# Optimization experiments

Measured on AMD Instinct MI355X. Metric: run time of the kernel, lower is better.

## Reference

```python
import jax, jax.numpy as jnp
import numpy as np

B, S, F, H = 64, 2048, 1024, 1024


def setup_inputs() -> dict:
    key = jax.random.key(0)
    k0, k1, k2, k3, k4 = jax.random.split(key, 5)
    scale = 1.0 / np.sqrt(H)
    return {
        "inputs": jax.random.normal(k0, (B, S, F), jnp.float32),
        "hidden_state": jnp.zeros((B, H), jnp.float32),
        "W_ih": jax.random.uniform(k1, (H, F), jnp.float32, -scale, scale),
        "W_hh": jax.random.uniform(k2, (H, H), jnp.float32, -scale, scale),
        "b_ih": jax.random.uniform(k3, (H,), jnp.float32, -scale, scale),
        "b_hh": jax.random.uniform(k4, (H,), jnp.float32, -scale, scale),
        "chunk_len": 128,
        "chunk_stride": 128,
    }


def reference(inputs, hidden_state, W_ih, W_hh, b_ih, b_hh, chunk_len, chunk_stride):
    # ReverseRNNLayer with chunk_stride == chunk_len and S % chunk_len == 0:
    # each chunk starts from a zeroed hidden state (incl. the first chunk) and is
    # scanned in reverse time order; outputs are collected per index then the
    # whole list is reversed, yielding chunks in reverse chunk order with
    # ascending time order inside each chunk.
    b_, S_, F_ = inputs.shape
    H_ = W_hh.shape[0]
    L = chunk_len
    NC = S_ // L
    # (B, NC, L, F) -> reversed time within chunk -> (L, B*NC, F)
    xc = inputs.reshape(b_, NC, L, F_)
    xr = jnp.flip(xc, axis=2).transpose(2, 0, 1, 3).reshape(L, b_ * NC, F_)
    # precompute input projection outside the scan (hoists the big GEMM)
    xproj = xr @ W_ih.T + (b_ih + b_hh)  # (L, B*NC, H)

    def step(h, xp):
        h = jnp.tanh(xp + h @ W_hh.T)
        return h, h

    h0 = jnp.zeros((b_ * NC, H_), inputs.dtype)
    h_last, ys = jax.lax.scan(step, h0, xproj)  # ys: (L, B*NC, H), reversed time
    ys = jnp.flip(ys, axis=0)                   # ascending time within chunk
    ys = ys.reshape(L, b_, NC, H_).transpose(1, 2, 0, 3)  # (B, NC, L, H)
    ys = jnp.flip(ys, axis=1).reshape(b_, S_, H_)  # chunks in reverse chunk order
    # final hidden state = carry after processing the LAST chunk
    h_final = h_last.reshape(b_, NC, H_)[:, NC - 1]
    return ys, h_final
```

## Files before the change

kernel.cpp:

```cpp
#include <hip/hip_runtime.h>
#include <hip/hip_bf16.h>
#include <stdint.h>

typedef __bf16 bf16x8 __attribute__((ext_vector_type(8)));
typedef float f32x4 __attribute__((ext_vector_type(4)));

#define Bb 64
#define Ss 2048
#define Ff 1024
#define Hh 1024
#define Ll 128
#define NCc 16

__device__ __forceinline__ uint16_t f2bf_rne(float x) {
    union { float f; uint32_t u; } c; c.f = x;
    uint32_t u = c.u;
    return (uint16_t)((u + 0x7FFFu + ((u >> 16) & 1u)) >> 16);
}

__device__ __forceinline__ void load_lds16(const void* g, void* l) {
    __builtin_amdgcn_global_load_lds(
        (__attribute__((address_space(1))) void*)(uintptr_t)g,
        (__attribute__((address_space(3))) void*)l, 16, 0, 0);
}

__global__ __launch_bounds__(256) void prep_kernel(
    const float* __restrict__ Wih, const float* __restrict__ Whh,
    const float* __restrict__ bih, const float* __restrict__ bhh,
    uint16_t* __restrict__ wih_bf, uint16_t* __restrict__ whh_bf,
    uint16_t* __restrict__ h0, float* __restrict__ bias,
    unsigned* __restrict__ bar)
{
    int i = blockIdx.x * 256 + threadIdx.x;
    wih_bf[i] = f2bf_rne(Wih[i]);
    whh_bf[i] = f2bf_rne(Whh[i]);
    h0[i] = 0;
    if (i < Hh) bias[i] = bih[i] + bhh[i];
    if (i < 1024) bar[i] = 0u;
}

__global__ __launch_bounds__(256) void xproj_kernel(
    const float* __restrict__ x, const uint16_t* __restrict__ wih,
    const float* __restrict__ bias, float* __restrict__ out)
{
    __shared__ __bf16 As[128*32];
    __shared__ __bf16 Bs[128*32];
    const int hb = blockIdx.y & 7;
    const int mb = blockIdx.x * 128 + (blockIdx.y >> 3);
    const int tid = threadIdx.x;
    const int wave = tid >> 6, lane = tid & 63;
    const int wm = (wave >> 1) * 64, wn = (wave & 1) * 64;

    const int t  = mb >> 3;
    const int n0 = (mb & 7) * 128;

    int arow[4], acol[4];
#pragma unroll
    for (int p = 0; p < 4; ++p) {
        int idx = p*256 + tid;
        int r = idx >> 3, c4 = idx & 7;
        int n = n0 + r;
        int b = n >> 4, c = n & 15;
        arow[p] = b*Ss + c*Ll + (Ll-1-t);
        acol[p] = c4*4;
    }

    f32x4 acc[4][4] = {};

    for (int k0 = 0; k0 < Ff; k0 += 32) {
        __syncthreads();
#pragma unroll
        for (int p = 0; p < 2; ++p) {
            int idx = p*256 + tid;
            int r = idx >> 2, c = idx & 3;
            load_lds16(wih + (size_t)(hb*128 + r)*1024 + (k0 + c*8), (char*)Bs + idx*16);
        }
#pragma unroll
        for (int p = 0; p < 4; ++p) {
            int idx = p*256 + tid;
            const float4 v = *(const float4*)(x + (size_t)arow[p]*Ff + k0 + acol[p]);
            uint32_t lo = (uint32_t)f2bf_rne(v.x) | ((uint32_t)f2bf_rne(v.y) << 16);
            uint32_t hi = (uint32_t)f2bf_rne(v.z) | ((uint32_t)f2bf_rne(v.w) << 16);
            *(uint2*)((char*)As + idx*8) = make_uint2(lo, hi);
        }
        __syncthreads();

        bf16x8 af[4], bfr[4];
#pragma unroll
        for (int i = 0; i < 4; ++i)
            af[i] = *(const bf16x8*)&As[(wm + i*16 + (lane & 15))*32 + (lane >> 4)*8];
#pragma unroll
        for (int j = 0; j < 4; ++j)
            bfr[j] = *(const bf16x8*)&Bs[(wn + j*16 + (lane & 15))*32 + (lane >> 4)*8];
#pragma unroll
        for (int i = 0; i < 4; ++i)
#pragma unroll
            for (int j = 0; j < 4; ++j)
                acc[i][j] = __builtin_amdgcn_mfma_f32_16x16x32_bf16(af[i], bfr[j], acc[i][j], 0, 0, 0);
    }

    float bsv[4]; int coln[4];
#pragma unroll
    for (int j = 0; j < 4; ++j) {
        coln[j] = hb*128 + wn + j*16 + (lane & 15);
        bsv[j] = bias[coln[j]];
    }
#pragma unroll
    for (int i = 0; i < 4; ++i) {
#pragma unroll
        for (int r = 0; r < 4; ++r) {
            int n = n0 + wm + i*16 + (lane >> 4)*4 + r;
            int b = n >> 4, c = n & 15;
            size_t orow = (size_t)b*Ss + (size_t)(NCc-1-c)*Ll + (Ll-1-t);
            float* orp = out + orow*Hh;
#pragma unroll
            for (int j = 0; j < 4; ++j)
                orp[coln[j]] = acc[i][j][r] + bsv[j];
        }
    }
}


__device__ __forceinline__ void stage_A(const uint16_t* __restrict__ hp, int nb, int c,
                                        __bf16* dst, int tid) {
#pragma unroll
    for (int p = 0; p < 2; ++p) {
        int u = p*256 + tid;
        int r = u >> 3;
        int s = u & 7;
        int k = (c << 6) + ((s ^ (r & 7)) << 3);
        load_lds16(hp + ((size_t)(nb*64 + r) << 10) + k, (char*)dst + u*16);
    }
}

__global__ __launch_bounds__(256, 1) void scan_kernel(
    const uint16_t* __restrict__ whh,
    uint16_t* __restrict__ h0buf, uint16_t* __restrict__ h1buf,
    float* __restrict__ out, unsigned* __restrict__ bar)
{
    __shared__ __align__(16) __bf16 Bs[64 * 1024];
    __shared__ __align__(16) __bf16 As[2][64 * 64];

    const int bid = blockIdx.x;
    const int nb = bid & 15;
    const int hb = bid >> 4;
    const int tid = threadIdx.x;
    const int lane = tid & 63;
    const int wave = tid >> 6;
    const int wm = (wave >> 1) * 32, wn = (wave & 1) * 32;
    const int l15 = lane & 15, l4 = lane >> 4;

    unsigned* cnt = bar + nb * 64;
    unsigned* gen = bar + nb * 64 + 32;

    for (int u = tid; u < 8192; u += 256) {
        int r = u >> 7, s = u & 127;
        int k = (s ^ (r & 7)) << 3;
        bf16x8 v = *(const bf16x8*)(whh + ((size_t)(hb*64 + r) << 10) + k);
        *(bf16x8*)((char*)Bs + u*16) = v;
    }

    float* orb[2][4];
    int hoff[2][4];
#pragma unroll
    for (int i = 0; i < 2; ++i)
#pragma unroll
        for (int r = 0; r < 4; ++r) {
            int n = nb*64 + wm + l4*4 + i*16 + r;
            int b = n >> 4, cch = n & 15;
            orb[i][r] = out + ((size_t)b*Ss + (size_t)(NCc-1-cch)*Ll)*Hh + hb*64;
            hoff[i][r] = n*Hh + hb*64;
        }

    __syncthreads();

#pragma unroll 1
    for (int t = 0; t < Ll; ++t) {
        const uint16_t* hp = (t & 1) ? h1buf : h0buf;
        uint16_t*       hn = (t & 1) ? h0buf : h1buf;
        const size_t toff = (size_t)(Ll-1-t) * Hh;

        float xpv[2][4][2];
#pragma unroll
        for (int i = 0; i < 2; ++i)
#pragma unroll
            for (int r = 0; r < 4; ++r) {
                const float* orp = orb[i][r] + toff;
                xpv[i][r][0] = orp[wn + l15];
                xpv[i][r][1] = orp[wn + 16 + l15];
            }

        f32x4 acc[2][2] = {};

        if (t > 0) {
            stage_A(hp, nb, 0, &As[0][0], tid);
            __syncthreads();
#pragma unroll
            for (int c = 0; c < 16; ++c) {
                if (c < 15) stage_A(hp, nb, c + 1, &As[(c + 1) & 1][0], tid);
                const char* Ab = (const char*)&As[c & 1][0];
#pragma unroll
                for (int ks = 0; ks < 2; ++ks) {
                    bf16x8 af[2], bv[2];
#pragma unroll
                    for (int i = 0; i < 2; ++i) {
                        int r = wm + i*16 + l15;
                        int off = r*128 + ((ks*64 + l4*16) ^ ((r & 7) << 4));
                        af[i] = *(const bf16x8*)(Ab + off);
                    }
#pragma unroll
                    for (int j = 0; j < 2; ++j) {
                        int r = wn + j*16 + l15;
                        int off = r*2048 + ((c*128 + ks*64 + l4*16) ^ ((r & 7) << 4));
                        bv[j] = *(const bf16x8*)((const char*)Bs + off);
                    }
#pragma unroll
                    for (int i = 0; i < 2; ++i)
#pragma unroll
                        for (int j = 0; j < 2; ++j)
                            acc[i][j] = __builtin_amdgcn_mfma_f32_16x16x32_bf16(af[i], bv[j], acc[i][j], 0, 0, 0);
                }
                __syncthreads();
            }
        }

#pragma unroll
        for (int i = 0; i < 2; ++i)
#pragma unroll
            for (int r = 0; r < 4; ++r) {
                float* orp = orb[i][r] + toff;
                uint16_t* hnp = hn + hoff[i][r];
#pragma unroll
                for (int j = 0; j < 2; ++j) {
                    int colo = wn + j*16 + l15;
                    float z = xpv[i][r][j] + acc[i][j][r];
                    float e = __expf(2.0f*z);
                    float h = 1.0f - 2.0f/(e + 1.0f);
                    orp[colo] = h;
                    hnp[colo] = f2bf_rne(h);
                    if (t == Ll-1 && r == 3 && l4 == 3) {
                        int b = (nb*64 + wm + i*16 + 15) >> 4;
                        out[(size_t)Bb*Ss*Hh + (size_t)b*Hh + hb*64 + colo] = h;
                    }
                }
            }

        if (t < Ll - 1) {
            __syncthreads();
            if (tid == 0) {
                unsigned g = __hip_atomic_load(gen, __ATOMIC_RELAXED, __HIP_MEMORY_SCOPE_AGENT);
                unsigned a = __hip_atomic_fetch_add(cnt, 1u, __ATOMIC_ACQ_REL, __HIP_MEMORY_SCOPE_AGENT);
                if (a == 15u) {
                    __hip_atomic_store(cnt, 0u, __ATOMIC_RELAXED, __HIP_MEMORY_SCOPE_AGENT);
                    __hip_atomic_store(gen, g + 1u, __ATOMIC_RELEASE, __HIP_MEMORY_SCOPE_AGENT);
                } else {
                    while (__hip_atomic_load(gen, __ATOMIC_RELAXED, __HIP_MEMORY_SCOPE_AGENT) == g)
                        __builtin_amdgcn_s_sleep(2);
                    (void)__hip_atomic_load(gen, __ATOMIC_ACQUIRE, __HIP_MEMORY_SCOPE_AGENT);
                }
            }
            __syncthreads();
        }
    }
}

extern "C" void kernel_launch(void* const* d_in, const int* in_sizes, int n_in,
                              void* d_out, int out_size, void* d_ws, size_t ws_size,
                              hipStream_t stream)
{
    const float* x   = (const float*)d_in[0];
    const float* Wih = (const float*)d_in[2];
    const float* Whh = (const float*)d_in[3];
    const float* bih = (const float*)d_in[4];
    const float* bhh = (const float*)d_in[5];
    float* out = (float*)d_out;

    char* ws = (char*)d_ws;
    uint16_t* wih_bf = (uint16_t*)(ws);
    uint16_t* whh_bf = (uint16_t*)(ws + (size_t)(2<<20));
    uint16_t* hb0    = (uint16_t*)(ws + (size_t)(4<<20));
    uint16_t* hb1    = (uint16_t*)(ws + (size_t)(6<<20));
    float*    bias   = (float*)(ws + (size_t)(8<<20));
    unsigned* bar    = (unsigned*)(ws + (size_t)(8<<20) + 4096);

    prep_kernel<<<4096, 256, 0, stream>>>(Wih, Whh, bih, bhh, wih_bf, whh_bf, hb0, bias, bar);
    xproj_kernel<<<dim3(8, 1024), 256, 0, stream>>>(x, wih_bf, bias, out);

    void* args[] = { (void*)&whh_bf, (void*)&hb0, (void*)&hb1, (void*)&out, (void*)&bar };
    hipLaunchCooperativeKernel(scan_kernel, dim3(256), dim3(256), args, 0, stream);
}
```

Measured before the change: 3.436 ms.

## Replace counter barrier with per-block flags, triple-buffer h staging, prefetch xproj

New measurement: 3.559 ms. 1.04x slower.

```diff
diff --git a/kernel.cpp b/kernel.cpp
--- a/kernel.cpp
+++ b/kernel.cpp
@@ -36,7 +36,7 @@
     whh_bf[i] = f2bf_rne(Whh[i]);
     h0[i] = 0;
     if (i < Hh) bias[i] = bih[i] + bhh[i];
-    if (i < 1024) bar[i] = 0u;
+    if (i < 4096) bar[i] = 0u;
 }
 
 __global__ __launch_bounds__(256) void xproj_kernel(
@@ -136,10 +136,10 @@
 __global__ __launch_bounds__(256, 1) void scan_kernel(
     const uint16_t* __restrict__ whh,
     uint16_t* __restrict__ h0buf, uint16_t* __restrict__ h1buf,
-    float* __restrict__ out, unsigned* __restrict__ bar)
+    float* __restrict__ out, unsigned* __restrict__ flags)
 {
     __shared__ __align__(16) __bf16 Bs[64 * 1024];
-    __shared__ __align__(16) __bf16 As[2][64 * 64];
+    __shared__ __align__(16) __bf16 As[3][64 * 64];
 
     const int bid = blockIdx.x;
     const int nb = bid & 15;
@@ -150,9 +150,6 @@
     const int wm = (wave >> 1) * 32, wn = (wave & 1) * 32;
     const int l15 = lane & 15, l4 = lane >> 4;
 
-    unsigned* cnt = bar + nb * 64;
-    unsigned* gen = bar + nb * 64 + 32;
-
     for (int u = tid; u < 8192; u += 256) {
         int r = u >> 7, s = u & 127;
         int k = (s ^ (r & 7)) << 3;
@@ -172,6 +169,19 @@
             hoff[i][r] = n*Hh + hb*64;
         }
 
+    float xq[2][4][2];
+    {
+        const size_t tf0 = (size_t)(Ll-1) * Hh;
+#pragma unroll
+        for (int i = 0; i < 2; ++i)
+#pragma unroll
+            for (int r = 0; r < 4; ++r) {
+                const float* orp = orb[i][r] + tf0;
+                xq[i][r][0] = orp[wn + l15];
+                xq[i][r][1] = orp[wn + 16 + l15];
+            }
+    }
+
     __syncthreads();
 
 #pragma unroll 1
@@ -180,25 +190,18 @@
         uint16_t*       hn = (t & 1) ? h0buf : h1buf;
         const size_t toff = (size_t)(Ll-1-t) * Hh;
 
-        float xpv[2][4][2];
-#pragma unroll
-        for (int i = 0; i < 2; ++i)
-#pragma unroll
-            for (int r = 0; r < 4; ++r) {
-                const float* orp = orb[i][r] + toff;
-                xpv[i][r][0] = orp[wn + l15];
-                xpv[i][r][1] = orp[wn + 16 + l15];
-            }
-
         f32x4 acc[2][2] = {};
 
         if (t > 0) {
             stage_A(hp, nb, 0, &As[0][0], tid);
-            __syncthreads();
+            stage_A(hp, nb, 1, &As[1][0], tid);
 #pragma unroll
             for (int c = 0; c < 16; ++c) {
-                if (c < 15) stage_A(hp, nb, c + 1, &As[(c + 1) & 1][0], tid);
-                const char* Ab = (const char*)&As[c & 1][0];
+                if (c < 15) { asm volatile("s_waitcnt vmcnt(2)" ::: "memory"); }
+                else        { asm volatile("s_waitcnt vmcnt(0)" ::: "memory"); }
+                __builtin_amdgcn_s_barrier();
+                if (c < 14) stage_A(hp, nb, c + 2, &As[(c + 2) % 3][0], tid);
+                const char* Ab = (const char*)&As[c % 3][0];
 #pragma unroll
                 for (int ks = 0; ks < 2; ++ks) {
                     bf16x8 af[2], bv[2];
@@ -220,7 +223,6 @@
                         for (int j = 0; j < 2; ++j)
                             acc[i][j] = __builtin_amdgcn_mfma_f32_16x16x32_bf16(af[i], bv[j], acc[i][j], 0, 0, 0);
                 }
-                __syncthreads();
             }
         }
 
@@ -233,7 +235,7 @@
 #pragma unroll
                 for (int j = 0; j < 2; ++j) {
                     int colo = wn + j*16 + l15;
-                    float z = xpv[i][r][j] + acc[i][j][r];
+                    float z = xq[i][r][j] + acc[i][j][r];
                     float e = __expf(2.0f*z);
                     float h = 1.0f - 2.0f/(e + 1.0f);
                     orp[colo] = h;
@@ -247,19 +249,39 @@
 
         if (t < Ll - 1) {
             __syncthreads();
-            if (tid == 0) {
-                unsigned g = __hip_atomic_load(gen, __ATOMIC_RELAXED, __HIP_MEMORY_SCOPE_AGENT);
-                unsigned a = __hip_atomic_fetch_add(cnt, 1u, __ATOMIC_ACQ_REL, __HIP_MEMORY_SCOPE_AGENT);
-                if (a == 15u) {
-                    __hip_atomic_store(cnt, 0u, __ATOMIC_RELAXED, __HIP_MEMORY_SCOPE_AGENT);
-                    __hip_atomic_store(gen, g + 1u, __ATOMIC_RELEASE, __HIP_MEMORY_SCOPE_AGENT);
-                } else {
-                    while (__hip_atomic_load(gen, __ATOMIC_RELAXED, __HIP_MEMORY_SCOPE_AGENT) == g)
-                        __builtin_amdgcn_s_sleep(2);
-                    (void)__hip_atomic_load(gen, __ATOMIC_ACQUIRE, __HIP_MEMORY_SCOPE_AGENT);
+            if (tid == 0)
+                __hip_atomic_store(flags + ((nb*16 + hb) << 4), (unsigned)(t + 1),
+                                   __ATOMIC_RELEASE, __HIP_MEMORY_SCOPE_AGENT);
+            float xq2[2][4][2];
+            {
+                const size_t tf2 = (size_t)(Ll-2-t) * Hh;
+#pragma unroll
+                for (int i = 0; i < 2; ++i)
+#pragma unroll
+                    for (int r = 0; r < 4; ++r) {
+                        const float* orp = orb[i][r] + tf2;
+                        xq2[i][r][0] = orp[wn + l15];
+                        xq2[i][r][1] = orp[wn + 16 + l15];
+                    }
+            }
+            if (tid < 64) {
+                unsigned* fp = flags + ((nb*16 + (tid & 15)) << 4);
+                while (true) {
+                    unsigned v = __hip_atomic_load(fp, __ATOMIC_RELAXED, __HIP_MEMORY_SCOPE_AGENT);
+                    if (!__ballot((tid < 16) && (v < (unsigned)(t + 1)))) break;
+                    __builtin_amdgcn_s_sleep(1);
                 }
+                if (tid == 0)
+                    (void)__hip_atomic_load(fp, __ATOMIC_ACQUIRE, __HIP_MEMORY_SCOPE_AGENT);
             }
             __syncthreads();
+#pragma unroll
+            for (int i = 0; i < 2; ++i)
+#pragma unroll
+                for (int r = 0; r < 4; ++r) {
+                    xq[i][r][0] = xq2[i][r][0];
+                    xq[i][r][1] = xq2[i][r][1];
+                }
         }
     }
 }
```
